# Kernel tuning notes

Hardware: AMD Instinct MI355X
Metric: run time of the kernel (lower is better)

Reference implementation:

```python
import jax, jax.numpy as jnp
import numpy as np

# 5x5 scent diffusion kernel (hard-coded in torch source)
SCENT_K = jnp.array([[0.0, 0.125, 0.25, 0.125, 0.0],
                     [0.125, 0.25, 0.5, 0.25, 0.125],
                     [0.25, 0.5, 1.0, 0.5, 0.25],
                     [0.125, 0.25, 0.5, 0.25, 0.125],
                     [0.0, 0.125, 0.25, 0.125, 0.0]], dtype=jnp.float32)
# Sobel-like perception kernels
DX = jnp.outer(jnp.array([1.0, 2.0, 1.0]), jnp.array([-1.0, 0.0, 1.0])) / 8.0
DY = DX.T


def _maxpool3(x):  # x: (H, W); 3x3 maxpool, stride 1, SAME padding
    return jax.lax.reduce_window(x, -jnp.inf, jax.lax.max, (3, 3), (1, 1), 'SAME')


def _depthwise3(x, k):  # x: (4, H, W); same 3x3 kernel applied per channel
    # treat channels as batch: (4,1,H,W) conv (1,1,3,3)
    return jax.lax.conv_general_dilated(x[:, None], k[None, None].astype(x.dtype),
                                        (1, 1), 'SAME')[:, 0]


def _update(cell, food, w3, b3, w4, b4):
    # scent: 5x5 conv on food (note: torch mutates cell[3] in place before masking)
    scent = jax.lax.conv_general_dilated(food[None, None], SCENT_K[None, None],
                                         (1, 1), 'SAME')[0, 0]
    cell = cell.at[3].set(scent)
    pre_alive = _maxpool3(cell[0]) > 0.1
    # perceive: (4 + 4 + 4) = 12 channels
    y = jnp.concatenate([cell, _depthwise3(cell, DX), _depthwise3(cell, DY)], axis=0)
    h = jax.nn.relu(jnp.einsum('oc,chw->ohw', w3, y) + b3[:, None, None])
    delta = jnp.einsum('oc,chw->ohw', w4, h) + b4[:, None, None]
    x = cell + delta
    post_alive = _maxpool3(x[0]) > 0.1
    mask = (pre_alive & post_alive).astype(x.dtype)
    x = x * mask
    x = x.at[3].set(cell[3])  # restore scent channel
    return jnp.clip(x, -10.0, 10.0)


def setup_inputs() -> dict:
    key = jax.random.key(0)
    k1, k2, k3, k4 = jax.random.split(key, 4)
    return {
        'cell': jax.random.normal(k1, (4, 17, 17), dtype=jnp.float32),
        'food': jax.random.uniform(k2, (17, 17), dtype=jnp.float32),
        'w3': jax.random.normal(k3, (16, 12), dtype=jnp.float32) * 0.1,
        'b3': jnp.zeros((16,), dtype=jnp.float32),
        'w4': jax.random.normal(k4, (4, 16), dtype=jnp.float32) * 0.1,
        'b4': jnp.zeros((4,), dtype=jnp.float32),
        'steps': 256,
    }


def reference(cell, food, w3, b3, w4, b4, steps):
    def step(c, _):
        return _update(c, food, w3, b3, w4, b4), None
    cell, _ = jax.lax.scan(step, cell, None, length=steps)
    living_count = jnp.sum(cell[0])
    return cell, food, living_count
```

## Files before the change

kernel.cpp:

```cpp
#include <hip/hip_runtime.h>

namespace {

constexpr int H = 17, W = 17, NC = H * W;
constexpr int SW = 20, SH = 19;
constexpr int NT = 320;

#define PIN(x) asm volatile("" : "+v"(x))

__device__ __forceinline__ float clip10(float v) {
    return fminf(fmaxf(v, -10.f), 10.f);
}

__device__ __forceinline__ float max3f(float a, float b, float c) {
    return fmaxf(fmaxf(a, b), c);
}

__device__ __forceinline__ float scent_at(int hy, int wx, const float* __restrict__ food) {
    const float SK[5][5] = {
        {0.f,   .125f, .25f, .125f, 0.f},
        {.125f, .25f,  .5f,  .25f,  .125f},
        {.25f,  .5f,   1.f,  .5f,   .25f},
        {.125f, .25f,  .5f,  .25f,  .125f},
        {0.f,   .125f, .25f, .125f, 0.f}};
    float sc = 0.f;
    #pragma unroll
    for (int dy = -2; dy <= 2; ++dy) {
        #pragma unroll
        for (int dx = -2; dx <= 2; ++dx) {
            const float k = SK[dy + 2][dx + 2];
            if (k != 0.f) {
                const int yy = hy + dy, xx = wx + dx;
                if (yy >= 0 && yy < H && xx >= 0 && xx < W)
                    sc = fmaf(k, food[yy * W + xx], sc);
            }
        }
    }
    return sc;
}

#define LOAD9(ARR, IDX, T)                                                        \
    const float T##00 = ARR[(IDX)-SW-1], T##01 = ARR[(IDX)-SW], T##02 = ARR[(IDX)-SW+1], \
                T##10 = ARR[(IDX)-1],    T##11 = ARR[(IDX)],    T##12 = ARR[(IDX)+1],    \
                T##20 = ARR[(IDX)+SW-1], T##21 = ARR[(IDX)+SW], T##22 = ARR[(IDX)+SW+1];

__launch_bounds__(NT, 2)
__global__ void ca_kernel(const float* __restrict__ cell_in,
                          const float* __restrict__ food,
                          const float* __restrict__ w3,
                          const float* __restrict__ b3,
                          const float* __restrict__ w4,
                          const float* __restrict__ b4,
                          const int* __restrict__ steps_p,
                          float* __restrict__ out)
{
    __shared__ float c0s[SH * SW];
    __shared__ float c1s[SH * SW];
    __shared__ float c2s[SH * SW];
    __shared__ float scs[SH * SW];
    __shared__ float xb[SH * SW];
    __shared__ float red[NT];

    const int tid = (int)threadIdx.x;
    const int steps = steps_p[0];
    const bool act = tid < NC;

    for (int i = tid; i < SH * SW; i += NT) {
        c0s[i] = 0.f; c1s[i] = 0.f; c2s[i] = 0.f; scs[i] = 0.f; xb[i] = 0.f;
    }
    __syncthreads();

    const int hy = act ? tid / W : 0;
    const int wx = act ? tid % W : 0;
    const int idx = (hy + 1) * SW + wx + 1;

    if (act) {
        c0s[idx] = cell_in[tid];
        c1s[idx] = cell_in[NC + tid];
        c2s[idx] = cell_in[2 * NC + tid];
        scs[idx] = scent_at(hy, wx, food);
    }
    __syncthreads();

    float wp[16][9];
    #pragma unroll
    for (int o = 0; o < 16; ++o) {
        wp[o][0] = w3[o*12 + 0];
        wp[o][1] = w3[o*12 + 1];
        wp[o][2] = w3[o*12 + 2];
        wp[o][3] = w3[o*12 + 4] * 0.125f;
        wp[o][4] = w3[o*12 + 5] * 0.125f;
        wp[o][5] = w3[o*12 + 6] * 0.125f;
        wp[o][6] = w3[o*12 + 8] * 0.125f;
        wp[o][7] = w3[o*12 + 9] * 0.125f;
        wp[o][8] = w3[o*12 + 10] * 0.125f;
    }
    float b40 = b4[0], b41 = b4[1], b42 = b4[2];

    float be[16];
    {
        LOAD9(scs, idx, s)
        const float dxs = ((s02-s00) + 2.f*(s12-s10) + (s22-s20)) * 0.125f;
        const float dys = ((s20+2.f*s21+s22) - (s00+2.f*s01+s02)) * 0.125f;
        #pragma unroll
        for (int o = 0; o < 16; ++o)
            be[o] = fmaf(w3[o*12+3], s11, fmaf(w3[o*12+7], dxs,
                    fmaf(w3[o*12+11], dys, b3[o])));
    }

    #pragma unroll
    for (int o = 0; o < 16; ++o) {
        #pragma unroll
        for (int c = 0; c < 9; ++c) PIN(wp[o][c]);
        PIN(be[o]);
    }
    PIN(b40); PIN(b41); PIN(b42);

    for (int s = 0; s < steps; ++s) {
        float n0 = 0.f, n1 = 0.f, n2 = 0.f;
        bool pre = false;
        if (act) {
            LOAD9(c0s, idx, p) LOAD9(c1s, idx, q) LOAD9(c2s, idx, r)
            const float y0 = p11, y1 = q11, y2 = r11;
            const float y3 = (p02-p00) + 2.f*(p12-p10) + (p22-p20);
            const float y4 = (q02-q00) + 2.f*(q12-q10) + (q22-q20);
            const float y5 = (r02-r00) + 2.f*(r12-r10) + (r22-r20);
            const float y6 = (p20+2.f*p21+p22) - (p00+2.f*p01+p02);
            const float y7 = (q20+2.f*q21+q22) - (q00+2.f*q01+q02);
            const float y8 = (r20+2.f*r21+r22) - (r00+2.f*r01+r02);
            pre = max3f(max3f(p00,p01,p02), max3f(p10,p11,p12),
                        max3f(p20,p21,p22)) > 0.1f;
            float d0 = b40, d1 = b41, d2 = b42;
            #pragma unroll
            for (int o = 0; o < 16; ++o) {
                float a = be[o];
                a = fmaf(wp[o][0], y0, a); a = fmaf(wp[o][1], y1, a);
                a = fmaf(wp[o][2], y2, a); a = fmaf(wp[o][3], y3, a);
                a = fmaf(wp[o][4], y4, a); a = fmaf(wp[o][5], y5, a);
                a = fmaf(wp[o][6], y6, a); a = fmaf(wp[o][7], y7, a);
                a = fmaf(wp[o][8], y8, a);
                a = fmaxf(a, 0.f);
                d0 = fmaf(w4[o],      a, d0);
                d1 = fmaf(w4[16 + o], a, d1);
                d2 = fmaf(w4[32 + o], a, d2);
            }
            n0 = y0 + d0; n1 = y1 + d1; n2 = y2 + d2;
            xb[idx] = n0;
        }
        __syncthreads();
        if (act) {
            const float x00 = xb[idx-SW-1], x01 = xb[idx-SW], x02 = xb[idx-SW+1];
            const float x10 = xb[idx-1],                      x12 = xb[idx+1];
            const float x20 = xb[idx+SW-1], x21 = xb[idx+SW], x22 = xb[idx+SW+1];
            const float mx2 = max3f(max3f(x00,x01,x02), max3f(x10,n0,x12),
                                    max3f(x20,x21,x22));
            const float m = (pre && (mx2 > 0.1f)) ? 1.f : 0.f;
            c0s[idx] = clip10(n0 * m);
            c1s[idx] = clip10(n1 * m);
            c2s[idx] = clip10(n2 * m);
        }
        __syncthreads();
    }

    if (act) {
        const float v0 = c0s[idx];
        out[tid]          = v0;
        out[NC + tid]     = c1s[idx];
        out[2 * NC + tid] = c2s[idx];
        out[3 * NC + tid] = clip10(scs[idx]);
        out[4 * NC + tid] = food[tid];
        red[tid] = v0;
    } else {
        red[tid] = 0.f;
    }
    __syncthreads();
    if (tid < 64) {
        float s2 = red[tid] + red[tid + 64] + red[tid + 128]
                 + red[tid + 192] + red[tid + 256];
        #pragma unroll
        for (int off = 32; off > 0; off >>= 1)
            s2 += __shfl_down(s2, off, 64);
        if (tid == 0) out[5 * NC] = s2;
    }
}

}

extern "C" void kernel_launch(void* const* d_in, const int* in_sizes, int n_in,
                              void* d_out, int out_size, void* d_ws, size_t ws_size,
                              hipStream_t stream) {
    const float* cell = (const float*)d_in[0];
    const float* food = (const float*)d_in[1];
    const float* w3   = (const float*)d_in[2];
    const float* b3   = (const float*)d_in[3];
    const float* w4   = (const float*)d_in[4];
    const float* b4   = (const float*)d_in[5];
    const int*   st   = (const int*)d_in[6];
    float* out = (float*)d_out;
    ca_kernel<<<1, NT, 0, stream>>>(cell, food, w3, b3, w4, b4, st, out);
}
```

Before: 287.4 us.

## Pack channels 0/1 as float2 in LDS, stream weights from LDS, keep center in registers

Interleaves cell channels 0 and 1 into one float2 shared array so each stencil neighbour needs one 64-bit LDS read instead of two 32-bit reads. The 144 pinned weight registers are dropped: the first-layer weights and the w4 columns are packed into float4s in shared memory and read with broadcast loads in the inner loop. Each thread's own cell values stay in registers across steps. This lowers LDS instruction count and register pressure, at the cost of extra LDS weight loads every step.

```diff
diff --git a/kernel.cpp b/kernel.cpp
--- a/kernel.cpp
+++ b/kernel.cpp
@@ -39,11 +39,6 @@
     return sc;
 }
 
-#define LOAD9(ARR, IDX, T)                                                        \
-    const float T##00 = ARR[(IDX)-SW-1], T##01 = ARR[(IDX)-SW], T##02 = ARR[(IDX)-SW+1], \
-                T##10 = ARR[(IDX)-1],    T##11 = ARR[(IDX)],    T##12 = ARR[(IDX)+1],    \
-                T##20 = ARR[(IDX)+SW-1], T##21 = ARR[(IDX)+SW], T##22 = ARR[(IDX)+SW+1];
-
 __launch_bounds__(NT, 2)
 __global__ void ca_kernel(const float* __restrict__ cell_in,
                           const float* __restrict__ food,
@@ -54,19 +49,27 @@
                           const int* __restrict__ steps_p,
                           float* __restrict__ out)
 {
-    __shared__ float c0s[SH * SW];
-    __shared__ float c1s[SH * SW];
-    __shared__ float c2s[SH * SW];
-    __shared__ float scs[SH * SW];
-    __shared__ float xb[SH * SW];
-    __shared__ float red[NT];
+    __shared__ float2 c01[SH * SW];
+    __shared__ float  c2s[SH * SW];
+    __shared__ float  scs[SH * SW];
+    __shared__ float  xb[SH * SW];
+    __shared__ float4 wlds[48];
+    __shared__ float  red[NT];
 
     const int tid = (int)threadIdx.x;
     const int steps = steps_p[0];
     const bool act = tid < NC;
 
     for (int i = tid; i < SH * SW; i += NT) {
-        c0s[i] = 0.f; c1s[i] = 0.f; c2s[i] = 0.f; scs[i] = 0.f; xb[i] = 0.f;
+        c01[i] = make_float2(0.f, 0.f);
+        c2s[i] = 0.f; scs[i] = 0.f; xb[i] = 0.f;
+    }
+    if (tid < 16) {
+        const int o = tid;
+        wlds[3*o]   = make_float4(w3[o*12+0], w3[o*12+1], w3[o*12+2], w3[o*12+4]*0.125f);
+        wlds[3*o+1] = make_float4(w3[o*12+5]*0.125f, w3[o*12+6]*0.125f,
+                                  w3[o*12+8]*0.125f, w3[o*12+9]*0.125f);
+        wlds[3*o+2] = make_float4(w3[o*12+10]*0.125f, w4[o], w4[16+o], w4[32+o]);
     }
     __syncthreads();
 
@@ -74,75 +77,70 @@
     const int wx = act ? tid % W : 0;
     const int idx = (hy + 1) * SW + wx + 1;
 
+    float cur0 = 0.f, cur1 = 0.f, cur2 = 0.f, sc = 0.f;
     if (act) {
-        c0s[idx] = cell_in[tid];
-        c1s[idx] = cell_in[NC + tid];
-        c2s[idx] = cell_in[2 * NC + tid];
-        scs[idx] = scent_at(hy, wx, food);
+        cur0 = cell_in[tid];
+        cur1 = cell_in[NC + tid];
+        cur2 = cell_in[2 * NC + tid];
+        sc   = scent_at(hy, wx, food);
+        c01[idx] = make_float2(cur0, cur1);
+        c2s[idx] = cur2;
+        scs[idx] = sc;
     }
     __syncthreads();
-
-    float wp[16][9];
-    #pragma unroll
-    for (int o = 0; o < 16; ++o) {
-        wp[o][0] = w3[o*12 + 0];
-        wp[o][1] = w3[o*12 + 1];
-        wp[o][2] = w3[o*12 + 2];
-        wp[o][3] = w3[o*12 + 4] * 0.125f;
-        wp[o][4] = w3[o*12 + 5] * 0.125f;
-        wp[o][5] = w3[o*12 + 6] * 0.125f;
-        wp[o][6] = w3[o*12 + 8] * 0.125f;
-        wp[o][7] = w3[o*12 + 9] * 0.125f;
-        wp[o][8] = w3[o*12 + 10] * 0.125f;
-    }
-    float b40 = b4[0], b41 = b4[1], b42 = b4[2];
 
     float be[16];
     {
-        LOAD9(scs, idx, s)
+        const float s00 = scs[idx-SW-1], s01 = scs[idx-SW], s02 = scs[idx-SW+1];
+        const float s10 = scs[idx-1],                       s12 = scs[idx+1];
+        const float s20 = scs[idx+SW-1], s21 = scs[idx+SW], s22 = scs[idx+SW+1];
         const float dxs = ((s02-s00) + 2.f*(s12-s10) + (s22-s20)) * 0.125f;
         const float dys = ((s20+2.f*s21+s22) - (s00+2.f*s01+s02)) * 0.125f;
         #pragma unroll
         for (int o = 0; o < 16; ++o)
-            be[o] = fmaf(w3[o*12+3], s11, fmaf(w3[o*12+7], dxs,
+            be[o] = fmaf(w3[o*12+3], sc, fmaf(w3[o*12+7], dxs,
                     fmaf(w3[o*12+11], dys, b3[o])));
     }
-
+    float b40 = b4[0], b41 = b4[1], b42 = b4[2];
     #pragma unroll
-    for (int o = 0; o < 16; ++o) {
-        #pragma unroll
-        for (int c = 0; c < 9; ++c) PIN(wp[o][c]);
-        PIN(be[o]);
-    }
+    for (int o = 0; o < 16; ++o) PIN(be[o]);
     PIN(b40); PIN(b41); PIN(b42);
 
     for (int s = 0; s < steps; ++s) {
         float n0 = 0.f, n1 = 0.f, n2 = 0.f;
         bool pre = false;
         if (act) {
-            LOAD9(c0s, idx, p) LOAD9(c1s, idx, q) LOAD9(c2s, idx, r)
-            const float y0 = p11, y1 = q11, y2 = r11;
-            const float y3 = (p02-p00) + 2.f*(p12-p10) + (p22-p20);
-            const float y4 = (q02-q00) + 2.f*(q12-q10) + (q22-q20);
+            const float2 a00 = c01[idx-SW-1], a01 = c01[idx-SW], a02 = c01[idx-SW+1];
+            const float2 a10 = c01[idx-1],                       a12 = c01[idx+1];
+            const float2 a20 = c01[idx+SW-1], a21 = c01[idx+SW], a22 = c01[idx+SW+1];
+            const float r00 = c2s[idx-SW-1], r01 = c2s[idx-SW], r02 = c2s[idx-SW+1];
+            const float r10 = c2s[idx-1],                       r12 = c2s[idx+1];
+            const float r20 = c2s[idx+SW-1], r21 = c2s[idx+SW], r22 = c2s[idx+SW+1];
+
+            const float y0 = cur0, y1 = cur1, y2 = cur2;
+            const float y3 = (a02.x-a00.x) + 2.f*(a12.x-a10.x) + (a22.x-a20.x);
+            const float y4 = (a02.y-a00.y) + 2.f*(a12.y-a10.y) + (a22.y-a20.y);
             const float y5 = (r02-r00) + 2.f*(r12-r10) + (r22-r20);
-            const float y6 = (p20+2.f*p21+p22) - (p00+2.f*p01+p02);
-            const float y7 = (q20+2.f*q21+q22) - (q00+2.f*q01+q02);
+            const float y6 = (a20.x+2.f*a21.x+a22.x) - (a00.x+2.f*a01.x+a02.x);
+            const float y7 = (a20.y+2.f*a21.y+a22.y) - (a00.y+2.f*a01.y+a02.y);
             const float y8 = (r20+2.f*r21+r22) - (r00+2.f*r01+r02);
-            pre = max3f(max3f(p00,p01,p02), max3f(p10,p11,p12),
-                        max3f(p20,p21,p22)) > 0.1f;
+            pre = max3f(max3f(a00.x,a01.x,a02.x), max3f(a10.x,cur0,a12.x),
+                        max3f(a20.x,a21.x,a22.x)) > 0.1f;
+
             float d0 = b40, d1 = b41, d2 = b42;
             #pragma unroll
             for (int o = 0; o < 16; ++o) {
+                const float4 wa = wlds[3*o], wb = wlds[3*o+1], wc = wlds[3*o+2];
                 float a = be[o];
-                a = fmaf(wp[o][0], y0, a); a = fmaf(wp[o][1], y1, a);
-                a = fmaf(wp[o][2], y2, a); a = fmaf(wp[o][3], y3, a);
-                a = fmaf(wp[o][4], y4, a); a = fmaf(wp[o][5], y5, a);
-                a = fmaf(wp[o][6], y6, a); a = fmaf(wp[o][7], y7, a);
-                a = fmaf(wp[o][8], y8, a);
+                a = fmaf(wa.x, y0, a); a = fmaf(wa.y, y1, a);
+                a = fmaf(wa.z, y2, a); a = fmaf(wa.w, y3, a);
+                a = fmaf(wb.x, y4, a); a = fmaf(wb.y, y5, a);
+                a = fmaf(wb.z, y6, a); a = fmaf(wb.w, y7, a);
+                a = fmaf(wc.x, y8, a);
                 a = fmaxf(a, 0.f);
-                d0 = fmaf(w4[o],      a, d0);
-                d1 = fmaf(w4[16 + o], a, d1);
-                d2 = fmaf(w4[32 + o], a, d2);
+                d0 = fmaf(wc.y, a, d0);
+                d1 = fmaf(wc.z, a, d1);
+                d2 = fmaf(wc.w, a, d2);
             }
             n0 = y0 + d0; n1 = y1 + d1; n2 = y2 + d2;
             xb[idx] = n0;
@@ -155,21 +153,22 @@
             const float mx2 = max3f(max3f(x00,x01,x02), max3f(x10,n0,x12),
                                     max3f(x20,x21,x22));
             const float m = (pre && (mx2 > 0.1f)) ? 1.f : 0.f;
-            c0s[idx] = clip10(n0 * m);
-            c1s[idx] = clip10(n1 * m);
-            c2s[idx] = clip10(n2 * m);
+            cur0 = clip10(n0 * m);
+            cur1 = clip10(n1 * m);
+            cur2 = clip10(n2 * m);
+            c01[idx] = make_float2(cur0, cur1);
+            c2s[idx] = cur2;
         }
         __syncthreads();
     }
 
     if (act) {
-        const float v0 = c0s[idx];
-        out[tid]          = v0;
-        out[NC + tid]     = c1s[idx];
-        out[2 * NC + tid] = c2s[idx];
-        out[3 * NC + tid] = clip10(scs[idx]);
+        out[tid]          = cur0;
+        out[NC + tid]     = cur1;
+        out[2 * NC + tid] = cur2;
+        out[3 * NC + tid] = clip10(sc);
         out[4 * NC + tid] = food[tid];
-        red[tid] = v0;
+        red[tid] = cur0;
     } else {
         red[tid] = 0.f;
     }
```

Result: slower. 355.3 us (+23.6%).
